# Kernel optimization log

Measured on AMD Instinct MI355X. Metric: run time of the kernel, lower is better.

Reference implementation:

```python
import jax, jax.numpy as jnp
import numpy as np

L, B, E = 128, 16, 512
C_OUT = 64
KERNELS = [1, 3, 5, 7]
M = len(KERNELS) * C_OUT          # mlpdec_in = 256
OUT_SIZE = 256
SLOPE = 0.1


def setup_inputs() -> dict:
    key = jax.random.key(0)
    ks = jax.random.split(key, 32)
    s = 0.02
    d = {"x": jax.random.normal(ks[0], (L, B, E), dtype=jnp.float32)}
    # conv branches: weight (C_out, 1, k, E), bias (C_out,)
    for i, k in enumerate(KERNELS):
        d[f"cw{i}"] = jax.random.normal(ks[1 + 2 * i], (C_OUT, 1, k, E), dtype=jnp.float32) * s
        d[f"cb{i}"] = jnp.zeros((C_OUT,), dtype=jnp.float32)
    dims = [(C_OUT, 2 * M), (C_OUT, C_OUT), (C_OUT, C_OUT), (C_OUT, C_OUT)]
    for i, (o, inn) in enumerate(dims):
        d[f"mw{i}"] = jax.random.normal(ks[10 + 2 * i], (o, inn), dtype=jnp.float32) * s
        d[f"mb{i}"] = jnp.zeros((o,), dtype=jnp.float32)
    # mlp_layer: Linear(C->C), Linear(C->output_size)
    d["lw0"] = jax.random.normal(ks[20], (C_OUT, C_OUT), dtype=jnp.float32) * s
    d["lb0"] = jnp.zeros((C_OUT,), dtype=jnp.float32)
    d["lw1"] = jax.random.normal(ks[21], (OUT_SIZE, C_OUT), dtype=jnp.float32) * s
    d["lb1"] = jnp.zeros((OUT_SIZE,), dtype=jnp.float32)
    return d


def _lrelu(x):
    return jax.nn.leaky_relu(x, SLOPE)


def _conv_branch(xb, w, b):
    # xb: (B,1,L,E), w: (C,1,k,E) -> (B,C,L)
    k = w.shape[2]
    pad = (k - 1) // 2
    y = jax.lax.conv_general_dilated(
        xb, w, window_strides=(1, 1), padding=[(pad, pad), (0, 0)],
        dimension_numbers=("NCHW", "OIHW", "NCHW"))
    return _lrelu(y[..., 0] + b[None, :, None])


def reference(x, cw0, cb0, cw1, cb1, cw2, cb2, cw3, cb3,
              mw0, mb0, mw1, mb1, mw2, mb2, mw3, mb3,
              lw0, lb0, lw1, lb1):
    # x: (L,B,E) -> (B,1,L,E)
    xb = jnp.transpose(x, (1, 0, 2))[:, None, :, :]
    feats = jnp.concatenate([
        _conv_branch(xb, cw0, cb0), _conv_branch(xb, cw1, cb1),
        _conv_branch(xb, cw2, cb2), _conv_branch(xb, cw3, cb3)], axis=1)  # (B, 4C, L)
    f = jnp.transpose(feats, (2, 0, 1))  # (L, B, M)
    # pairwise: pair[i, j] = [f[j], f[i]]  -> (L, L, B, 2M)
    a = jnp.broadcast_to(f[None, :, :, :], (L, L, B, M))
    bpart = jnp.broadcast_to(f[:, None, :, :], (L, L, B, M))
    h = jnp.concatenate([a, bpart], axis=-1)
    for w, bb in ((mw0, mb0), (mw1, mb1), (mw2, mb2), (mw3, mb3)):
        h = _lrelu(h @ w.T + bb)
    h = h.sum(axis=0)  # (L, B, C)
    h = _lrelu(h @ lw0.T + lb0)
    return _lrelu(h @ lw1.T + lb1)  # (L, B, OUT_SIZE)
```

## Files before the change

### kernel.cpp

```cpp
#include <hip/hip_runtime.h>
#include <hip/hip_bf16.h>

#define SLOPE 0.1f
typedef unsigned short u16;
typedef unsigned int u32;
typedef __attribute__((ext_vector_type(8))) short short8;
typedef __attribute__((ext_vector_type(4))) float floatx4;

__device__ __forceinline__ float lrelu(float x) { return x > 0.0f ? x : SLOPE * x; }

__device__ __forceinline__ void split_rn(float x, u16* h, u16* l) {
    union { __hip_bfloat16 b; u16 u; } c1, c2;
    c1.b = __float2bfloat16(x);
    float hf = __bfloat162float(c1.b);
    c2.b = __float2bfloat16(x - hf);
    *h = c1.u; *l = c2.u;
}

__device__ __forceinline__ void pack2x2(float v0, float v1, u32& h, u32& l) {
    u32 a0 = __float_as_uint(v0), a1 = __float_as_uint(v1);
    h = __builtin_amdgcn_perm(a1, a0, 0x07060302u);
    float r0 = v0 - __uint_as_float(a0 & 0xFFFF0000u);
    float r1 = v1 - __uint_as_float(a1 & 0xFFFF0000u);
    l = __builtin_amdgcn_perm(__float_as_uint(r1), __float_as_uint(r0), 0x07060302u);
}

__device__ __forceinline__ short8 load_frag(const u16* p) {
    union { uint4 q; short8 s; } cv;
    cv.q = *(const uint4*)p;
    return cv.s;
}

__device__ __forceinline__ floatx4 mfma16(short8 a, short8 b, floatx4 c) {
    return __builtin_amdgcn_mfma_f32_16x16x32_bf16(a, b, c, 0, 0, 0);
}

__global__ __launch_bounds__(256) void p0_prep(
    const float* __restrict__ x,
    const float* __restrict__ cw0, const float* __restrict__ cw1,
    const float* __restrict__ cw2, const float* __restrict__ cw3,
    const float* __restrict__ mw0, const float* __restrict__ mw1,
    const float* __restrict__ mw2, const float* __restrict__ mw3,
    const float* __restrict__ lw0, const float* __restrict__ lw1,
    u16* __restrict__ xfh, u16* __restrict__ xfl,
    u16* __restrict__ wcfh, u16* __restrict__ wcfl,
    u16* __restrict__ b2fh, u16* __restrict__ b2fl,
    u16* __restrict__ w3fh, u16* __restrict__ w3fl,
    float* __restrict__ lw0t, float* __restrict__ lw1t)
{
    int idx = (blockIdx.x * 256 + threadIdx.x) * 4;
    if (idx < 1048576) {
        const int j = idx & 7, lane = (idx >> 3) & 63;
        const int kc = (idx >> 9) & 15, rt = idx >> 13;
        const int l15 = lane & 15, quad = lane >> 4;
        const float4 s = *(const float4*)(x + (rt * 16 + l15) * 512 + kc * 32 + quad * 8 + j);
        u16 h[4], l[4];
        split_rn(s.x, &h[0], &l[0]); split_rn(s.y, &h[1], &l[1]);
        split_rn(s.z, &h[2], &l[2]); split_rn(s.w, &h[3], &l[3]);
        *(ushort4*)(xfh + idx) = make_ushort4(h[0], h[1], h[2], h[3]);
        *(ushort4*)(xfl + idx) = make_ushort4(l[0], l[1], l[2], l[3]);
        return;
    }
    idx -= 1048576;
    if (idx < 524288) {
        const int j = idx & 7, lane = (idx >> 3) & 63;
        const int kc = (idx >> 9) & 15, nt = (idx >> 13) & 3, slot = idx >> 15;
        int branch, base;
        if (slot == 0)      { branch = 0; base = 0; }
        else if (slot < 4)  { branch = 1; base = 1; }
        else if (slot < 9)  { branch = 2; base = 4; }
        else                { branch = 3; base = 9; }
        const int dk = slot - base, ksz = 2 * branch + 1;
        const float* cw = branch == 0 ? cw0 : branch == 1 ? cw1 : branch == 2 ? cw2 : cw3;
        const int c = nt * 16 + (lane & 15);
        const int e = kc * 32 + (lane >> 4) * 8 + j;
        const float4 s = *(const float4*)(cw + (c * ksz + dk) * 512 + e);
        u16 h[4], l[4];
        split_rn(s.x, &h[0], &l[0]); split_rn(s.y, &h[1], &l[1]);
        split_rn(s.z, &h[2], &l[2]); split_rn(s.w, &h[3], &l[3]);
        *(ushort4*)(wcfh + idx) = make_ushort4(h[0], h[1], h[2], h[3]);
        *(ushort4*)(wcfl + idx) = make_ushort4(l[0], l[1], l[2], l[3]);
        return;
    }
    idx -= 524288;
    if (idx < 32768) {
        const int j = idx & 7, lane = (idx >> 3) & 63;
        const int kc = (idx >> 9) & 7, nt = (idx >> 12) & 3, nh = idx >> 14;
        const int n = nh * 64 + nt * 16 + (lane & 15);
        const int k = kc * 32 + (lane >> 4) * 8 + j;
        const float4 s = *(const float4*)(mw0 + (n & 63) * 512 + (n >> 6) * 256 + k);
        u16 h[4], l[4];
        split_rn(s.x, &h[0], &l[0]); split_rn(s.y, &h[1], &l[1]);
        split_rn(s.z, &h[2], &l[2]); split_rn(s.w, &h[3], &l[3]);
        *(ushort4*)(b2fh + idx) = make_ushort4(h[0], h[1], h[2], h[3]);
        *(ushort4*)(b2fl + idx) = make_ushort4(l[0], l[1], l[2], l[3]);
        return;
    }
    idx -= 32768;
    if (idx < 12288) {
        const int j = idx & 7, lane = (idx >> 3) & 63;
        const int kc = (idx >> 9) & 1, mt = (idx >> 10) & 3, layer = idx >> 12;
        const float* mw = layer == 0 ? mw1 : layer == 1 ? mw2 : mw3;
        const int ch = mt * 16 + (lane & 15);
        const int k = kc * 32 + (lane >> 4) * 8 + j;
        const float4 s = *(const float4*)(mw + ch * 64 + k);
        u16 h[4], l[4];
        split_rn(s.x, &h[0], &l[0]); split_rn(s.y, &h[1], &l[1]);
        split_rn(s.z, &h[2], &l[2]); split_rn(s.w, &h[3], &l[3]);
        *(ushort4*)(w3fh + idx) = make_ushort4(h[0], h[1], h[2], h[3]);
        *(ushort4*)(w3fl + idx) = make_ushort4(l[0], l[1], l[2], l[3]);
        return;
    }
    idx -= 12288;
    if (idx < 4096) {
        const int k = idx >> 6, n = idx & 63;
        float4 o;
        o.x = lw0[(n + 0) * 64 + k]; o.y = lw0[(n + 1) * 64 + k];
        o.z = lw0[(n + 2) * 64 + k]; o.w = lw0[(n + 3) * 64 + k];
        *(float4*)(lw0t + idx) = o;
        return;
    }
    idx -= 4096;
    if (idx < 16384) {
        const int k = idx >> 8, n = idx & 255;
        float4 o;
        o.x = lw1[(n + 0) * 64 + k]; o.y = lw1[(n + 1) * 64 + k];
        o.z = lw1[(n + 2) * 64 + k]; o.w = lw1[(n + 3) * 64 + k];
        *(float4*)(lw1t + idx) = o;
        return;
    }
}

__global__ __launch_bounds__(512) void k1f_conv(
    const u16* __restrict__ xfh, const u16* __restrict__ xfl,
    const u16* __restrict__ wcfh, const u16* __restrict__ wcfl,
    const float* __restrict__ cb0, const float* __restrict__ cb1,
    const float* __restrict__ cb2, const float* __restrict__ cb3,
    u16* __restrict__ Ffh, u16* __restrict__ Ffl)
{
    __shared__ float P[8][16][72];

    const int t = threadIdx.x, lane = t & 63, w = t >> 6;
    const int rtp = blockIdx.x;
    const int br = blockIdx.y;
    const int base = br * br;
    const int ksz = 2 * br + 1;
    const int l15 = lane & 15, quad = lane >> 4;

    floatx4 acc[2][4];
    #pragma unroll
    for (int r = 0; r < 2; ++r)
        #pragma unroll
        for (int j = 0; j < 4; ++j) acc[r][j] = (floatx4)0.0f;

    const int nunits = ksz * 16;
    for (int unit = w; unit < nunits; unit += 8) {
        const int dk = unit >> 4, kc = unit & 15;
        const int slot = base + dk;
        short8 bh[4], bl[4];
        #pragma unroll
        for (int nt = 0; nt < 4; ++nt) {
            const int boff = (((slot * 4 + nt) * 16 + kc) * 64 + lane) * 8;
            bh[nt] = load_frag(wcfh + boff);
            bl[nt] = load_frag(wcfl + boff);
        }
        #pragma unroll
        for (int r = 0; r < 2; ++r) {
            const int rts = rtp + r * 64 + dk - br;
            if (rts < 0 || rts >= 128) continue;
            const int aoff = ((rts * 16 + kc) * 64 + lane) * 8;
            const short8 ah = load_frag(xfh + aoff);
            const short8 al = load_frag(xfl + aoff);
            #pragma unroll
            for (int nt = 0; nt < 4; ++nt) {
                acc[r][nt] = mfma16(ah, bh[nt], acc[r][nt]);
                acc[r][nt] = mfma16(ah, bl[nt], acc[r][nt]);
                acc[r][nt] = mfma16(al, bh[nt], acc[r][nt]);
            }
        }
    }

    const float* cb = br == 0 ? cb0 : br == 1 ? cb1 : br == 2 ? cb2 : cb3;
    #pragma unroll
    for (int r = 0; r < 2; ++r) {
        #pragma unroll
        for (int nt = 0; nt < 4; ++nt)
            #pragma unroll
            for (int rr = 0; rr < 4; ++rr)
                P[w][quad * 4 + rr][nt * 16 + l15] = acc[r][nt][rr];
        __syncthreads();
        if (t < 256) {
            const int row = t >> 4, c4 = (t & 15) * 4;
            u16 h4[4], l4[4];
            #pragma unroll
            for (int i = 0; i < 4; ++i) {
                float val = cb[c4 + i];
                #pragma unroll
                for (int ww = 0; ww < 8; ++ww) val += P[ww][row][c4 + i];
                split_rn(lrelu(val), &h4[i], &l4[i]);
            }
            const int rt = rtp + r * 64;
            const int m4 = br * 64 + c4;
            const int dst = ((rt * 8 + (m4 >> 5)) * 64 + ((m4 >> 3) & 3) * 16 + row) * 8 + (m4 & 7);
            *(ushort4*)(Ffh + dst) = make_ushort4(h4[0], h4[1], h4[2], h4[3]);
            *(ushort4*)(Ffl + dst) = make_ushort4(l4[0], l4[1], l4[2], l4[3]);
        }
        __syncthreads();
    }
}

__global__ __launch_bounds__(256) void k2_uv(
    const u16* __restrict__ Ffh, const u16* __restrict__ Ffl,
    const u16* __restrict__ b2fh, const u16* __restrict__ b2fl,
    const float* __restrict__ mb0,
    float* __restrict__ u, float* __restrict__ v_t)
{
    __shared__ float P[4][16][72];

    const int t = threadIdx.x, lane = t & 63, w = t >> 6;
    const int rt = blockIdx.x;
    const int nh = blockIdx.y;
    const int l15 = lane & 15, quad = lane >> 4;

    floatx4 acc[4];
    #pragma unroll
    for (int j = 0; j < 4; ++j) acc[j] = (floatx4)0.0f;

    #pragma unroll
    for (int kk = 0; kk < 2; ++kk) {
        const int kc = w * 2 + kk;
        const int aoff = ((rt * 8 + kc) * 64 + lane) * 8;
        const short8 ah = load_frag(Ffh + aoff);
        const short8 al = load_frag(Ffl + aoff);
        #pragma unroll
        for (int nt = 0; nt < 4; ++nt) {
            const int boff = (((nh * 4 + nt) * 8 + kc) * 64 + lane) * 8;
            const short8 bh = load_frag(b2fh + boff);
            const short8 bl = load_frag(b2fl + boff);
            acc[nt] = mfma16(ah, bh, acc[nt]);
            acc[nt] = mfma16(ah, bl, acc[nt]);
            acc[nt] = mfma16(al, bh, acc[nt]);
        }
    }

    #pragma unroll
    for (int nt = 0; nt < 4; ++nt)
        #pragma unroll
        for (int r = 0; r < 4; ++r)
            P[w][quad * 4 + r][nt * 16 + l15] = acc[nt][r];
    __syncthreads();

    const int row = t >> 4, c4 = (t & 15) * 4;
    const int rglob = rt * 16 + row;
    float4 oo;
    #pragma unroll
    for (int i = 0; i < 4; ++i)
        (&oo.x)[i] = P[0][row][c4 + i] + P[1][row][c4 + i]
                   + P[2][row][c4 + i] + P[3][row][c4 + i];
    if (nh == 0) {
        oo.x += mb0[c4 + 0]; oo.y += mb0[c4 + 1];
        oo.z += mb0[c4 + 2]; oo.w += mb0[c4 + 3];
        *(float4*)(u + rglob * 64 + c4) = oo;
    } else {
        const int i = rglob >> 4, b = rglob & 15;
        *(float4*)(v_t + (b * 128 + i) * 64 + c4) = oo;
    }
}

__global__ __launch_bounds__(256, 4) void k3_pair(
    const float* __restrict__ u, const float* __restrict__ v_t,
    const u16* __restrict__ w3fh, const u16* __restrict__ w3fl,
    const float* __restrict__ mb1, const float* __restrict__ mb2,
    const float* __restrict__ mb3,
    float* __restrict__ Spart)
{
    __shared__ __align__(16) u16 Hh[128][72];
    __shared__ __align__(16) u16 Hl[128][72];

    const int t = threadIdx.x, lane = t & 63, w = t >> 6;
    const int jb = blockIdx.x, b = jb & 15;
    const int l15 = lane & 15, quad = lane >> 4;
    const int i0 = w * 32;
    const int c4 = l15 * 4;

    const float4 uu = *(const float4*)(u + jb * 64 + c4);

    const float* vb = v_t + (b * 128 + i0) * 64;
    #pragma unroll
    for (int n = 0; n < 8; ++n) {
        const int idx = n * 64 + lane;
        const int il = idx >> 4;
        const float4 vv = *(const float4*)(vb + idx * 4);
        const float a0 = lrelu(vv.x + uu.x), a1 = lrelu(vv.y + uu.y);
        const float a2 = lrelu(vv.z + uu.z), a3 = lrelu(vv.w + uu.w);
        u32 h01, l01, h23, l23;
        pack2x2(a0, a1, h01, l01);
        pack2x2(a2, a3, h23, l23);
        *(uint2*)&Hh[i0 + il][c4] = make_uint2(h01, h23);
        *(uint2*)&Hl[i0 + il][c4] = make_uint2(l01, l23);
    }

    const float* mbp[3] = {mb1, mb2, mb3};
    for (int layer = 0; layer < 3; ++layer) {
        floatx4 acc[4][2];
        #pragma unroll
        for (int i = 0; i < 4; ++i)
            #pragma unroll
            for (int j = 0; j < 2; ++j) acc[i][j] = (floatx4)0.0f;

        #pragma unroll
        for (int kc = 0; kc < 2; ++kc) {
            short8 ah[4], al[4];
            #pragma unroll
            for (int mt = 0; mt < 4; ++mt) {
                const int aoff = (((layer * 4 + mt) * 2 + kc) * 64 + lane) * 8;
                ah[mt] = load_frag(w3fh + aoff);
                al[mt] = load_frag(w3fl + aoff);
            }
            const int k0 = kc * 32 + quad * 8;
            #pragma unroll
            for (int nt = 0; nt < 2; ++nt) {
                const short8 bh = load_frag(&Hh[i0 + nt * 16 + l15][k0]);
                const short8 bl = load_frag(&Hl[i0 + nt * 16 + l15][k0]);
                #pragma unroll
                for (int mt = 0; mt < 4; ++mt) {
                    acc[mt][nt] = mfma16(ah[mt], bh, acc[mt][nt]);
                    acc[mt][nt] = mfma16(ah[mt], bl, acc[mt][nt]);
                    acc[mt][nt] = mfma16(al[mt], bh, acc[mt][nt]);
                }
            }
        }

        if (layer < 2) {
            #pragma unroll
            for (int mt = 0; mt < 4; ++mt) {
                float bias[4];
                #pragma unroll
                for (int r = 0; r < 4; ++r) bias[r] = mbp[layer][mt * 16 + quad * 4 + r];
                #pragma unroll
                for (int nt = 0; nt < 2; ++nt) {
                    const int i = i0 + nt * 16 + l15;
                    const float v0 = lrelu(acc[mt][nt][0] + bias[0]);
                    const float v1 = lrelu(acc[mt][nt][1] + bias[1]);
                    const float v2 = lrelu(acc[mt][nt][2] + bias[2]);
                    const float v3 = lrelu(acc[mt][nt][3] + bias[3]);
                    u32 h01, l01, h23, l23;
                    pack2x2(v0, v1, h01, l01);
                    pack2x2(v2, v3, h23, l23);
                    *(uint2*)&Hh[i][mt * 16 + quad * 4] = make_uint2(h01, h23);
                    *(uint2*)&Hl[i][mt * 16 + quad * 4] = make_uint2(l01, l23);
                }
            }
        } else {
            #pragma unroll
            for (int mt = 0; mt < 4; ++mt) {
                float bias[4];
                #pragma unroll
                for (int r = 0; r < 4; ++r) bias[r] = mbp[2][mt * 16 + quad * 4 + r];
                float4 sv;
                #pragma unroll
                for (int r = 0; r < 4; ++r) {
                    float val = lrelu(acc[mt][0][r] + bias[r])
                              + lrelu(acc[mt][1][r] + bias[r]);
                    val += __shfl_xor(val, 1, 16);
                    val += __shfl_xor(val, 2, 16);
                    val += __shfl_xor(val, 4, 16);
                    val += __shfl_xor(val, 8, 16);
                    (&sv.x)[r] = val;
                }
                if (l15 == 0)
                    *(float4*)(Spart + jb * 256 + w * 64 + mt * 16 + quad * 4) = sv;
            }
        }
    }
}

__global__ __launch_bounds__(256) void k4_head(
    const float* __restrict__ Spart,
    const float* __restrict__ lw0t, const float* __restrict__ lb0,
    const float* __restrict__ lw1t, const float* __restrict__ lb1,
    float* __restrict__ out)
{
    __shared__ float Ss[8][64];
    __shared__ float T1[8][64];

    const int t = threadIdx.x;
    const int jb0 = blockIdx.x * 8;

    #pragma unroll
    for (int p = 0; p < 2; ++p) {
        const int idx = t + 256 * p;
        const int jbb = idx >> 6, ch = idx & 63;
        const float* sp = Spart + (jb0 + jbb) * 256 + ch;
        Ss[jbb][ch] = sp[0] + sp[64] + sp[128] + sp[192];
    }
    __syncthreads();

    #pragma unroll
    for (int p = 0; p < 2; ++p) {
        const int idx = t + 256 * p;
        const int jbb = idx >> 6, c = idx & 63;
        float a = lb0[c];
        #pragma unroll 8
        for (int k = 0; k < 64; ++k) a += Ss[jbb][k] * lw0t[k * 64 + c];
        T1[jbb][c] = lrelu(a);
    }
    __syncthreads();

    const int c = t;
    float acc[8];
    const float base = lb1[c];
    #pragma unroll
    for (int jbb = 0; jbb < 8; ++jbb) acc[jbb] = base;
    #pragma unroll 4
    for (int k = 0; k < 64; ++k) {
        const float wv = lw1t[k * 256 + c];
        #pragma unroll
        for (int jbb = 0; jbb < 8; ++jbb) acc[jbb] += T1[jbb][k] * wv;
    }
    #pragma unroll
    for (int jbb = 0; jbb < 8; ++jbb)
        out[(jb0 + jbb) * 256 + c] = lrelu(acc[jbb]);
}

extern "C" void kernel_launch(void* const* d_in, const int* in_sizes, int n_in,
                              void* d_out, int out_size, void* d_ws, size_t ws_size,
                              hipStream_t stream)
{
    const float* x   = (const float*)d_in[0];
    const float* cw0 = (const float*)d_in[1];
    const float* cb0 = (const float*)d_in[2];
    const float* cw1 = (const float*)d_in[3];
    const float* cb1 = (const float*)d_in[4];
    const float* cw2 = (const float*)d_in[5];
    const float* cb2 = (const float*)d_in[6];
    const float* cw3 = (const float*)d_in[7];
    const float* cb3 = (const float*)d_in[8];
    const float* mw0 = (const float*)d_in[9];
    const float* mb0 = (const float*)d_in[10];
    const float* mw1 = (const float*)d_in[11];
    const float* mb1 = (const float*)d_in[12];
    const float* mw2 = (const float*)d_in[13];
    const float* mb2 = (const float*)d_in[14];
    const float* mw3 = (const float*)d_in[15];
    const float* mb3 = (const float*)d_in[16];
    const float* lw0 = (const float*)d_in[17];
    const float* lb0 = (const float*)d_in[18];
    const float* lw1 = (const float*)d_in[19];
    const float* lb1 = (const float*)d_in[20];
    float* out = (float*)d_out;

    char* base = (char*)d_ws;
    u16* xfh   = (u16*)(base + 0);
    u16* xfl   = (u16*)(base + 2097152);
    u16* wcfh  = (u16*)(base + 4194304);
    u16* wcfl  = (u16*)(base + 5242880);
    u16* b2fh  = (u16*)(base + 6291456);
    u16* b2fl  = (u16*)(base + 6356992);
    u16* w3fh  = (u16*)(base + 6422528);
    u16* w3fl  = (u16*)(base + 6447104);
    float* lw0t  = (float*)(base + 6471680);
    float* lw1t  = (float*)(base + 6488064);
    u16* Ffh   = (u16*)(base + 6553600);
    u16* Ffl   = (u16*)(base + 7602176);
    float* u   = (float*)(base + 8650752);
    float* v_t = (float*)(base + 9175040);
    float* Spart = (float*)(base + 9699328);

    hipLaunchKernelGGL(p0_prep, dim3(1600), dim3(256), 0, stream,
                       x, cw0, cw1, cw2, cw3, mw0, mw1, mw2, mw3, lw0, lw1,
                       xfh, xfl, wcfh, wcfl, b2fh, b2fl, w3fh, w3fl, lw0t, lw1t);
    hipLaunchKernelGGL(k1f_conv, dim3(64, 4), dim3(512), 0, stream,
                       xfh, xfl, wcfh, wcfl, cb0, cb1, cb2, cb3, Ffh, Ffl);
    hipLaunchKernelGGL(k2_uv, dim3(128, 2), dim3(256), 0, stream,
                       Ffh, Ffl, b2fh, b2fl, mb0, u, v_t);
    hipLaunchKernelGGL(k3_pair, dim3(2048), dim3(256), 0, stream,
                       u, v_t, w3fh, w3fl, mb1, mb2, mb3, Spart);
    hipLaunchKernelGGL(k4_head, dim3(256), dim3(256), 0, stream,
                       Spart, lw0t, lb0, lw1t, lb1, out);
}
```

Before: 156.8 us.

## Fuse head MLP into pair kernel and rebalance conv branch work split

The head MLP (two small linears) now runs as an epilogue of k3_pair, one block per output row, so the separate k4_head launch and the Spart round trip through global memory go away. The conv kernel is regridded to 128x2 blocks: one half computes branches k=1,3,5 (9 taps) and the other computes k=7 (7 taps). This replaces the old per-branch split, where the tap counts 1/3/5/7 were uneven across blocks. In exchange, each k3 block does extra serial head work with only 64 active threads, and the conv blocks no longer reuse weight fragments across two row tiles.

```diff
diff --git a/kernel.cpp b/kernel.cpp
--- a/kernel.cpp
+++ b/kernel.cpp
@@ -141,71 +141,110 @@
     __shared__ float P[8][16][72];
 
     const int t = threadIdx.x, lane = t & 63, w = t >> 6;
-    const int rtp = blockIdx.x;
-    const int br = blockIdx.y;
-    const int base = br * br;
-    const int ksz = 2 * br + 1;
+    const int rt = blockIdx.x;
+    const int half = blockIdx.y;
     const int l15 = lane & 15, quad = lane >> 4;
-
-    floatx4 acc[2][4];
-    #pragma unroll
-    for (int r = 0; r < 2; ++r)
-        #pragma unroll
-        for (int j = 0; j < 4; ++j) acc[r][j] = (floatx4)0.0f;
-
-    const int nunits = ksz * 16;
-    for (int unit = w; unit < nunits; unit += 8) {
-        const int dk = unit >> 4, kc = unit & 15;
-        const int slot = base + dk;
-        short8 bh[4], bl[4];
-        #pragma unroll
-        for (int nt = 0; nt < 4; ++nt) {
-            const int boff = (((slot * 4 + nt) * 16 + kc) * 64 + lane) * 8;
-            bh[nt] = load_frag(wcfh + boff);
-            bl[nt] = load_frag(wcfl + boff);
-        }
-        #pragma unroll
-        for (int r = 0; r < 2; ++r) {
-            const int rts = rtp + r * 64 + dk - br;
+    const int row = (t & 255) >> 4, c4 = (t & 15) * 4;
+
+    if (half == 0) {
+        floatx4 acc[3][4];
+        #pragma unroll
+        for (int br = 0; br < 3; ++br)
+            #pragma unroll
+            for (int j = 0; j < 4; ++j) acc[br][j] = (floatx4)0.0f;
+
+        #pragma unroll
+        for (int br = 0; br < 3; ++br) {
+            const int base = br * br, ksz = 2 * br + 1;
+            for (int unit = w; unit < ksz * 16; unit += 8) {
+                const int dk = unit >> 4, kc = unit & 15;
+                const int rts = rt + dk - br;
+                if (rts < 0 || rts >= 128) continue;
+                const int slot = base + dk;
+                const int aoff = ((rts * 16 + kc) * 64 + lane) * 8;
+                const short8 ah = load_frag(xfh + aoff);
+                const short8 al = load_frag(xfl + aoff);
+                #pragma unroll
+                for (int nt = 0; nt < 4; ++nt) {
+                    const int boff = (((slot * 4 + nt) * 16 + kc) * 64 + lane) * 8;
+                    const short8 bh = load_frag(wcfh + boff);
+                    const short8 bl = load_frag(wcfl + boff);
+                    acc[br][nt] = mfma16(ah, bh, acc[br][nt]);
+                    acc[br][nt] = mfma16(ah, bl, acc[br][nt]);
+                    acc[br][nt] = mfma16(al, bh, acc[br][nt]);
+                }
+            }
+        }
+
+        #pragma unroll
+        for (int br = 0; br < 3; ++br) {
+            #pragma unroll
+            for (int nt = 0; nt < 4; ++nt)
+                #pragma unroll
+                for (int rr = 0; rr < 4; ++rr)
+                    P[w][quad * 4 + rr][nt * 16 + l15] = acc[br][nt][rr];
+            __syncthreads();
+            if (t < 256) {
+                const float* cb = br == 0 ? cb0 : br == 1 ? cb1 : cb2;
+                u16 h4[4], l4[4];
+                #pragma unroll
+                for (int i = 0; i < 4; ++i) {
+                    float val = cb[c4 + i];
+                    #pragma unroll
+                    for (int ww = 0; ww < 8; ++ww) val += P[ww][row][c4 + i];
+                    split_rn(lrelu(val), &h4[i], &l4[i]);
+                }
+                const int m4 = br * 64 + c4;
+                const int dst = ((rt * 8 + (m4 >> 5)) * 64 + ((m4 >> 3) & 3) * 16 + row) * 8 + (m4 & 7);
+                *(ushort4*)(Ffh + dst) = make_ushort4(h4[0], h4[1], h4[2], h4[3]);
+                *(ushort4*)(Ffl + dst) = make_ushort4(l4[0], l4[1], l4[2], l4[3]);
+            }
+            __syncthreads();
+        }
+    } else {
+        floatx4 acc[4];
+        #pragma unroll
+        for (int j = 0; j < 4; ++j) acc[j] = (floatx4)0.0f;
+
+        for (int unit = w; unit < 112; unit += 8) {
+            const int dk = unit >> 4, kc = unit & 15;
+            const int rts = rt + dk - 3;
             if (rts < 0 || rts >= 128) continue;
+            const int slot = 9 + dk;
             const int aoff = ((rts * 16 + kc) * 64 + lane) * 8;
             const short8 ah = load_frag(xfh + aoff);
             const short8 al = load_frag(xfl + aoff);
             #pragma unroll
             for (int nt = 0; nt < 4; ++nt) {
-                acc[r][nt] = mfma16(ah, bh[nt], acc[r][nt]);
-                acc[r][nt] = mfma16(ah, bl[nt], acc[r][nt]);
-                acc[r][nt] = mfma16(al, bh[nt], acc[r][nt]);
-            }
-        }
-    }
-
-    const float* cb = br == 0 ? cb0 : br == 1 ? cb1 : br == 2 ? cb2 : cb3;
-    #pragma unroll
-    for (int r = 0; r < 2; ++r) {
+                const int boff = (((slot * 4 + nt) * 16 + kc) * 64 + lane) * 8;
+                const short8 bh = load_frag(wcfh + boff);
+                const short8 bl = load_frag(wcfl + boff);
+                acc[nt] = mfma16(ah, bh, acc[nt]);
+                acc[nt] = mfma16(ah, bl, acc[nt]);
+                acc[nt] = mfma16(al, bh, acc[nt]);
+            }
+        }
+
         #pragma unroll
         for (int nt = 0; nt < 4; ++nt)
             #pragma unroll
             for (int rr = 0; rr < 4; ++rr)
-                P[w][quad * 4 + rr][nt * 16 + l15] = acc[r][nt][rr];
+                P[w][quad * 4 + rr][nt * 16 + l15] = acc[nt][rr];
         __syncthreads();
         if (t < 256) {
-            const int row = t >> 4, c4 = (t & 15) * 4;
             u16 h4[4], l4[4];
             #pragma unroll
             for (int i = 0; i < 4; ++i) {
-                float val = cb[c4 + i];
+                float val = cb3[c4 + i];
                 #pragma unroll
                 for (int ww = 0; ww < 8; ++ww) val += P[ww][row][c4 + i];
                 split_rn(lrelu(val), &h4[i], &l4[i]);
             }
-            const int rt = rtp + r * 64;
-            const int m4 = br * 64 + c4;
+            const int m4 = 192 + c4;
             const int dst = ((rt * 8 + (m4 >> 5)) * 64 + ((m4 >> 3) & 3) * 16 + row) * 8 + (m4 & 7);
             *(ushort4*)(Ffh + dst) = make_ushort4(h4[0], h4[1], h4[2], h4[3]);
             *(ushort4*)(Ffl + dst) = make_ushort4(l4[0], l4[1], l4[2], l4[3]);
         }
-        __syncthreads();
     }
 }
 
@@ -272,10 +311,15 @@
     const u16* __restrict__ w3fh, const u16* __restrict__ w3fl,
     const float* __restrict__ mb1, const float* __restrict__ mb2,
     const float* __restrict__ mb3,
-    float* __restrict__ Spart)
+    const float* __restrict__ lw0t, const float* __restrict__ lb0,
+    const float* __restrict__ lw1t, const float* __restrict__ lb1,
+    float* __restrict__ out)
 {
     __shared__ __align__(16) u16 Hh[128][72];
     __shared__ __align__(16) u16 Hl[128][72];
+    __shared__ float Sp[4][64];
+    __shared__ float Ss[64];
+    __shared__ float T1[64];
 
     const int t = threadIdx.x, lane = t & 63, w = t >> 6;
     const int jb = blockIdx.x, b = jb & 15;
@@ -369,58 +413,27 @@
                     (&sv.x)[r] = val;
                 }
                 if (l15 == 0)
-                    *(float4*)(Spart + jb * 256 + w * 64 + mt * 16 + quad * 4) = sv;
-            }
-        }
-    }
-}
-
-__global__ __launch_bounds__(256) void k4_head(
-    const float* __restrict__ Spart,
-    const float* __restrict__ lw0t, const float* __restrict__ lb0,
-    const float* __restrict__ lw1t, const float* __restrict__ lb1,
-    float* __restrict__ out)
-{
-    __shared__ float Ss[8][64];
-    __shared__ float T1[8][64];
-
-    const int t = threadIdx.x;
-    const int jb0 = blockIdx.x * 8;
-
-    #pragma unroll
-    for (int p = 0; p < 2; ++p) {
-        const int idx = t + 256 * p;
-        const int jbb = idx >> 6, ch = idx & 63;
-        const float* sp = Spart + (jb0 + jbb) * 256 + ch;
-        Ss[jbb][ch] = sp[0] + sp[64] + sp[128] + sp[192];
-    }
+                    *(float4*)(&Sp[w][mt * 16 + quad * 4]) = sv;
+            }
+        }
+    }
+
     __syncthreads();
-
-    #pragma unroll
-    for (int p = 0; p < 2; ++p) {
-        const int idx = t + 256 * p;
-        const int jbb = idx >> 6, c = idx & 63;
-        float a = lb0[c];
+    if (t < 64) Ss[t] = Sp[0][t] + Sp[1][t] + Sp[2][t] + Sp[3][t];
+    __syncthreads();
+    if (t < 64) {
+        float a = lb0[t];
         #pragma unroll 8
-        for (int k = 0; k < 64; ++k) a += Ss[jbb][k] * lw0t[k * 64 + c];
-        T1[jbb][c] = lrelu(a);
+        for (int k = 0; k < 64; ++k) a += Ss[k] * lw0t[k * 64 + t];
+        T1[t] = lrelu(a);
     }
     __syncthreads();
-
-    const int c = t;
-    float acc[8];
-    const float base = lb1[c];
-    #pragma unroll
-    for (int jbb = 0; jbb < 8; ++jbb) acc[jbb] = base;
-    #pragma unroll 4
-    for (int k = 0; k < 64; ++k) {
-        const float wv = lw1t[k * 256 + c];
-        #pragma unroll
-        for (int jbb = 0; jbb < 8; ++jbb) acc[jbb] += T1[jbb][k] * wv;
-    }
-    #pragma unroll
-    for (int jbb = 0; jbb < 8; ++jbb)
-        out[(jb0 + jbb) * 256 + c] = lrelu(acc[jbb]);
+    {
+        float a = lb1[t];
+        #pragma unroll 8
+        for (int k = 0; k < 64; ++k) a += T1[k] * lw1t[k * 256 + t];
+        out[jb * 256 + t] = lrelu(a);
+    }
 }
 
 extern "C" void kernel_launch(void* const* d_in, const int* in_sizes, int n_in,
@@ -465,17 +478,14 @@
     u16* Ffl   = (u16*)(base + 7602176);
     float* u   = (float*)(base + 8650752);
     float* v_t = (float*)(base + 9175040);
-    float* Spart = (float*)(base + 9699328);
 
     hipLaunchKernelGGL(p0_prep, dim3(1600), dim3(256), 0, stream,
                        x, cw0, cw1, cw2, cw3, mw0, mw1, mw2, mw3, lw0, lw1,
                        xfh, xfl, wcfh, wcfl, b2fh, b2fl, w3fh, w3fl, lw0t, lw1t);
-    hipLaunchKernelGGL(k1f_conv, dim3(64, 4), dim3(512), 0, stream,
+    hipLaunchKernelGGL(k1f_conv, dim3(128, 2), dim3(512), 0, stream,
                        xfh, xfl, wcfh, wcfl, cb0, cb1, cb2, cb3, Ffh, Ffl);
     hipLaunchKernelGGL(k2_uv, dim3(128, 2), dim3(256), 0, stream,
                        Ffh, Ffl, b2fh, b2fl, mb0, u, v_t);
     hipLaunchKernelGGL(k3_pair, dim3(2048), dim3(256), 0, stream,
-                       u, v_t, w3fh, w3fl, mb1, mb2, mb3, Spart);
-    hipLaunchKernelGGL(k4_head, dim3(256), dim3(256), 0, stream,
-                       Spart, lw0t, lb0, lw1t, lb1, out);
-}
+                       u, v_t, w3fh, w3fl, mb1, mb2, mb3, lw0t, lb0, lw1t, lb1, out);
+}
```

Measured after the change: 161.9 us. +3.3%, slower.
